# Kernel optimization log

Measured on AMD Instinct MI355X. Metric: run time of the kernel, lower is better.

Reference implementation:

```python
import jax, jax.numpy as jnp
import numpy as np

B = 2048
TT_IN = (16, 16, 16)    # prod = 4096
TT_OUT = (16, 16, 16)   # prod = 4096
BOND = (32, 32)
INIT_STD = 0.05  # keras 'random_normal' default stddev


def setup_inputs() -> dict:
    key = jax.random.key(0)
    k_x, k1, k2, k3 = jax.random.split(key, 4)
    x = jax.random.normal(k_x, (B, int(np.prod(TT_IN))), dtype=jnp.float32)
    core1 = jax.random.normal(k1, (TT_IN[0], TT_OUT[0], BOND[0]), dtype=jnp.float32) * INIT_STD
    core2 = jax.random.normal(k2, (TT_IN[1], TT_OUT[1], BOND[0], BOND[1]), dtype=jnp.float32) * INIT_STD
    core3 = jax.random.normal(k3, (TT_IN[2], TT_OUT[2], BOND[1]), dtype=jnp.float32) * INIT_STD
    bias = jnp.zeros(TT_OUT, dtype=jnp.float32)
    return {"x": x, "core1": core1, "core2": core2, "core3": core3, "bias": bias}


def reference(x, core1, core2, core3, bias):
    # x: [B, 4096] -> [B, x, y, z] tensor-train input modes
    xt = x.reshape((x.shape[0],) + TT_IN)
    # TT contraction: modes x,y,z contracted with cores; a,b,c are output
    # modes; p,q are bond indices (matches original einsum structure for
    # 3 cores: x[1,2,3], c1[1,4,7], c2[2,5,7,8], c3[3,6,8] -> [4,5,6]).
    out = jnp.einsum('nxyz,xap,ybpq,zcq->nabc', xt, core1, core2, core3,
                     optimize='optimal')
    out = out + bias  # bias broadcast over batch, shape TT_OUT
    out = out.reshape(x.shape[0], -1)  # [B, prod(TT_OUT)]
    return jax.nn.relu(out)
```

## Files before the change

kernel.cpp:

```cpp
#include <hip/hip_runtime.h>
#include <hip/hip_bf16.h>
#include <stdint.h>


typedef short bf16x8 __attribute__((ext_vector_type(8)));
typedef float f32x4  __attribute__((ext_vector_type(4)));

#define MB 2048
#define KD 4096
#define ND 4096
#define NT_K 64

__device__ __forceinline__ unsigned short f32_bf16(float f) {
  union { float f; uint32_t u; } v; v.f = f;
  return (unsigned short)((v.u + 0x7fffu + ((v.u >> 16) & 1u)) >> 16);
}
__device__ __forceinline__ float bf2f(unsigned short u) {
  union { uint32_t i; float f; } v; v.i = ((uint32_t)u) << 16; return v.f;
}

__global__ void k_conv(const float* __restrict__ x, unsigned short* __restrict__ xb) {
  int i = blockIdx.x * 256 + threadIdx.x;
  const float4* x4 = (const float4*)x;
  float4 a = x4[2*i];
  float4 b = x4[2*i+1];
  ushort4 lo, hi;
  lo.x = f32_bf16(a.x); lo.y = f32_bf16(a.y); lo.z = f32_bf16(a.z); lo.w = f32_bf16(a.w);
  hi.x = f32_bf16(b.x); hi.y = f32_bf16(b.y); hi.z = f32_bf16(b.z); hi.w = f32_bf16(b.w);
  ushort4* o = (ushort4*)xb;
  o[2*i]   = lo;
  o[2*i+1] = hi;
}

__global__ __launch_bounds__(256) void k_wt(const float* __restrict__ c1,
                                            const float* __restrict__ c2,
                                            const float* __restrict__ c3,
                                            unsigned short* __restrict__ Wt) {
  __shared__ unsigned short sh[17472];
  int ab = blockIdx.x;
  int t = threadIdx.x;
  int a = ab >> 4, b = ab & 15;
  unsigned short* c2s = sh;
  float* c1s = (float*)(sh + 16448);

  #pragma unroll
  for (int y = 0; y < 16; ++y) {
    float4 v = *(const float4*)(c2 + (size_t)(y*16 + b)*1024 + t*4);
    ushort4 s;
    s.x = f32_bf16(v.x); s.y = f32_bf16(v.y); s.z = f32_bf16(v.z); s.w = f32_bf16(v.w);
    *(ushort4*)(c2s + y*1028 + t*4) = s;
  }
  c1s[t]       = c1[((t>>5)*16 + a)*32 + (t&31)];
  c1s[t+256]   = c1[(((t>>5)+8)*16 + a)*32 + (t&31)];
  __syncthreads();

  int xx = t >> 4, yy = t & 15;
  const float* c1r = c1s + xx*32;
  const unsigned short* c2r = c2s + yy*1028;
  float acc[32];
  #pragma unroll
  for (int q = 0; q < 32; ++q) acc[q] = 0.f;
  #pragma unroll 8
  for (int p = 0; p < 32; ++p) {
    float w = c1r[p];
    #pragma unroll
    for (int j = 0; j < 8; ++j) {
      ushort4 v = *(const ushort4*)(c2r + p*32 + j*4);
      acc[4*j+0] = fmaf(w, bf2f(v.x), acc[4*j+0]);
      acc[4*j+1] = fmaf(w, bf2f(v.y), acc[4*j+1]);
      acc[4*j+2] = fmaf(w, bf2f(v.z), acc[4*j+2]);
      acc[4*j+3] = fmaf(w, bf2f(v.w), acc[4*j+3]);
    }
  }
  __syncthreads();

  unsigned short* T2s  = sh;
  unsigned short* c3ps = sh + 8192;

  #pragma unroll
  for (int j = 0; j < 8; ++j) {
    ushort4 s;
    s.x = f32_bf16(acc[4*j+0]); s.y = f32_bf16(acc[4*j+1]);
    s.z = f32_bf16(acc[4*j+2]); s.w = f32_bf16(acc[4*j+3]);
    *(ushort4*)(T2s + t*32 + j*4) = s;
  }
  #pragma unroll
  for (int r = 0; r < 8; ++r) {
    int i4 = t*8 + r;
    float4 v = *(const float4*)(c3 + (size_t)i4*4);
    int e = i4*4;
    int q = e & 31, zc = e >> 5;
    int z = zc >> 4, c = zc & 15;
    ushort4 s;
    s.x = f32_bf16(v.x); s.y = f32_bf16(v.y); s.z = f32_bf16(v.z); s.w = f32_bf16(v.w);
    *(ushort4*)(c3ps + (c*16 + z)*32 + q) = s;
  }
  __syncthreads();

  int wid = t >> 6, lane = t & 63, l15 = lane & 15, lg = lane >> 4;
  bf16x8 bfv[16];
  #pragma unroll
  for (int nt = 0; nt < 16; ++nt)
    bfv[nt] = *(const bf16x8*)(c3ps + (nt*16 + l15)*32 + lg*8);
  #pragma unroll
  for (int mi = 0; mi < 4; ++mi) {
    int mtile = wid*4 + mi;
    bf16x8 af = *(const bf16x8*)(T2s + (mtile*16 + l15)*32 + lg*8);
    #pragma unroll
    for (int nt = 0; nt < 16; ++nt) {
      f32x4 d = {0.f, 0.f, 0.f, 0.f};
      d = __builtin_amdgcn_mfma_f32_16x16x32_bf16(af, bfv[nt], d, 0, 0, 0);
      size_t jrow = (size_t)(ab*16 + nt) * ND;
      #pragma unroll
      for (int i = 0; i < 4; ++i) {
        int xy = mtile*16 + lg*4 + i;
        Wt[jrow + xy*16 + l15] = f32_bf16(d[i]);
      }
    }
  }
}

__device__ __forceinline__ void gload_lds16(const unsigned short* g, unsigned short* l) {
  __builtin_amdgcn_global_load_lds(
      (const __attribute__((address_space(1))) void*)g,
      (__attribute__((address_space(3))) void*)l, 16, 0, 0);
}

__global__ __launch_bounds__(512, 1) void k_gemm(const unsigned short* __restrict__ A,
                                                 const unsigned short* __restrict__ Bw,
                                                 const float* __restrict__ bias,
                                                 float* __restrict__ C) {
  __shared__ unsigned short As[3*128*64];
  __shared__ unsigned short Bs[3*256*64];
  const int t = threadIdx.x;
  const int wid = t >> 6, lane = t & 63;
  const int l15 = lane & 15, lg = lane >> 4;
  const int m0 = blockIdx.y * 128;
  const int n0 = blockIdx.x * 256;
  const int wr = wid >> 2, wc = wid & 3;
  const int xr = l15 & 7;

  const int scol = (((t & 7) ^ ((t >> 3) & 7)) * 8);
  const int t8 = t * 8;
  const unsigned short* Ag = A  + (size_t)(m0 + (t >> 3))*KD + scol;
  const unsigned short* Bg = Bw + (size_t)(n0 + (t >> 3))*KD + scol;

#define STG_A(tk, buf, s) gload_lds16(Ag + (size_t)(s)*64*KD + (tk)*64, \
                                      As + (buf)*8192  + (s)*4096 + t8)
#define STG_B(tk, buf, s) gload_lds16(Bg + (size_t)(s)*64*KD + (tk)*64, \
                                      Bs + (buf)*16384 + (s)*4096 + t8)

  f32x4 acc[4][4];
  #pragma unroll
  for (int m = 0; m < 4; ++m)
    #pragma unroll
    for (int n = 0; n < 4; ++n)
      acc[m][n] = (f32x4){0.f, 0.f, 0.f, 0.f};

  STG_A(0,0,0); STG_A(0,0,1); STG_B(0,0,0); STG_B(0,0,1); STG_B(0,0,2); STG_B(0,0,3);
  STG_A(1,1,0); STG_A(1,1,1); STG_B(1,1,0); STG_B(1,1,1); STG_B(1,1,2); STG_B(1,1,3);
  asm volatile("s_waitcnt vmcnt(6)" ::: "memory");
  __builtin_amdgcn_s_barrier();

  int cur = 0, stg = 2;
  for (int i = 0; i < NT_K; ++i) {
    const unsigned short* Ac = As + cur*8192;
    const unsigned short* Bc = Bs + cur*16384;
    const int  tk2 = i + 2;
    const bool do_stage = (i < NT_K - 2);
    bf16x8 aF[4], bF[4];

    {
      const int pc8 = ((0*4 + lg) ^ xr) * 8;
      #pragma unroll
      for (int m = 0; m < 4; ++m)
        aF[m] = *(const bf16x8*)(Ac + (wr*64 + m*16 + l15)*64 + pc8);
      #pragma unroll
      for (int n = 0; n < 4; ++n)
        bF[n] = *(const bf16x8*)(Bc + (wc*64 + n*16 + l15)*64 + pc8);
    }
    if (do_stage) { STG_A(tk2, stg, 0); STG_A(tk2, stg, 1); STG_B(tk2, stg, 0); }
    __builtin_amdgcn_s_barrier();
    asm volatile("s_waitcnt lgkmcnt(0)" ::: "memory");
    __builtin_amdgcn_sched_barrier(0);
    __builtin_amdgcn_s_setprio(1);
    #pragma unroll
    for (int m = 0; m < 4; ++m)
      #pragma unroll
      for (int n = 0; n < 4; ++n)
        acc[m][n] = __builtin_amdgcn_mfma_f32_16x16x32_bf16(aF[m], bF[n], acc[m][n], 0, 0, 0);
    __builtin_amdgcn_s_setprio(0);
    __builtin_amdgcn_s_barrier();

    {
      const int pc8 = ((1*4 + lg) ^ xr) * 8;
      #pragma unroll
      for (int m = 0; m < 4; ++m)
        aF[m] = *(const bf16x8*)(Ac + (wr*64 + m*16 + l15)*64 + pc8);
      #pragma unroll
      for (int n = 0; n < 4; ++n)
        bF[n] = *(const bf16x8*)(Bc + (wc*64 + n*16 + l15)*64 + pc8);
    }
    if (do_stage) { STG_B(tk2, stg, 1); STG_B(tk2, stg, 2); STG_B(tk2, stg, 3); }
    __builtin_amdgcn_s_barrier();
    asm volatile("s_waitcnt lgkmcnt(0)" ::: "memory");
    __builtin_amdgcn_sched_barrier(0);
    __builtin_amdgcn_s_setprio(1);
    #pragma unroll
    for (int m = 0; m < 4; ++m)
      #pragma unroll
      for (int n = 0; n < 4; ++n)
        acc[m][n] = __builtin_amdgcn_mfma_f32_16x16x32_bf16(aF[m], bF[n], acc[m][n], 0, 0, 0);
    __builtin_amdgcn_s_setprio(0);

    if (i < NT_K - 2)       { asm volatile("s_waitcnt vmcnt(6)" ::: "memory"); }
    else if (i == NT_K - 2) { asm volatile("s_waitcnt vmcnt(0)" ::: "memory"); }
    __builtin_amdgcn_s_barrier();

    cur = (cur == 2) ? 0 : cur + 1;
    stg = (stg == 2) ? 0 : stg + 1;
  }

  #pragma unroll
  for (int m = 0; m < 4; ++m) {
    int gr = m0 + wr*64 + m*16 + lg*4;
    #pragma unroll
    for (int n = 0; n < 4; ++n) {
      int gc = n0 + wc*64 + n*16 + l15;
      float bv = bias[gc];
      #pragma unroll
      for (int i = 0; i < 4; ++i) {
        float v = acc[m][n][i] + bv;
        C[(size_t)(gr + i)*ND + gc] = v > 0.f ? v : 0.f;
      }
    }
  }
#undef STG_A
#undef STG_B
}

extern "C" void kernel_launch(void* const* d_in, const int* in_sizes, int n_in,
                              void* d_out, int out_size, void* d_ws, size_t ws_size,
                              hipStream_t stream) {
  (void)in_sizes; (void)n_in; (void)out_size; (void)ws_size;
  const float* x    = (const float*)d_in[0];
  const float* c1   = (const float*)d_in[1];
  const float* c2   = (const float*)d_in[2];
  const float* c3   = (const float*)d_in[3];
  const float* bias = (const float*)d_in[4];
  float* out = (float*)d_out;

  uint8_t* ws = (uint8_t*)d_ws;
  unsigned short* xb = (unsigned short*)(ws);
  unsigned short* Wt = (unsigned short*)(ws + 16777216);

  k_conv<<<4096, 256, 0, stream>>>(x, xb);
  k_wt  <<<256,  256, 0, stream>>>(c1, c2, c3, Wt);
  k_gemm<<<dim3(ND/256, MB/128), 512, 0, stream>>>(xb, Wt, bias, out);
}
```

Baseline: 171.7 us.

## Split K across wave pairs in GEMM with LDS reduction of partial sums

```diff
diff --git a/kernel.cpp b/kernel.cpp
--- a/kernel.cpp
+++ b/kernel.cpp
@@ -130,14 +130,16 @@
                                                  const unsigned short* __restrict__ Bw,
                                                  const float* __restrict__ bias,
                                                  float* __restrict__ C) {
-  __shared__ unsigned short As[3*128*64];
-  __shared__ unsigned short Bs[3*256*64];
+  __shared__ uint8_t sh[147456];
+  unsigned short* As = (unsigned short*)sh;
+  unsigned short* Bs = (unsigned short*)(sh + 49152);
   const int t = threadIdx.x;
   const int wid = t >> 6, lane = t & 63;
   const int l15 = lane & 15, lg = lane >> 4;
   const int m0 = blockIdx.y * 128;
   const int n0 = blockIdx.x * 256;
-  const int wr = wid >> 2, wc = wid & 3;
+  const int wc  = wid & 3;
+  const int kkw = wid >> 2;
   const int xr = l15 & 7;
 
   const int scol = (((t & 7) ^ ((t >> 3) & 7)) * 8);
@@ -150,9 +152,9 @@
 #define STG_B(tk, buf, s) gload_lds16(Bg + (size_t)(s)*64*KD + (tk)*64, \
                                       Bs + (buf)*16384 + (s)*4096 + t8)
 
-  f32x4 acc[4][4];
-  #pragma unroll
-  for (int m = 0; m < 4; ++m)
+  f32x4 acc[8][4];
+  #pragma unroll
+  for (int m = 0; m < 8; ++m)
     #pragma unroll
     for (int n = 0; n < 4; ++n)
       acc[m][n] = (f32x4){0.f, 0.f, 0.f, 0.f};
@@ -162,76 +164,66 @@
   asm volatile("s_waitcnt vmcnt(6)" ::: "memory");
   __builtin_amdgcn_s_barrier();
 
+  const int pc8 = ((kkw*4 + lg) ^ xr) * 8;
+
   int cur = 0, stg = 2;
   for (int i = 0; i < NT_K; ++i) {
     const unsigned short* Ac = As + cur*8192;
     const unsigned short* Bc = Bs + cur*16384;
-    const int  tk2 = i + 2;
-    const bool do_stage = (i < NT_K - 2);
-    bf16x8 aF[4], bF[4];
-
-    {
-      const int pc8 = ((0*4 + lg) ^ xr) * 8;
-      #pragma unroll
-      for (int m = 0; m < 4; ++m)
-        aF[m] = *(const bf16x8*)(Ac + (wr*64 + m*16 + l15)*64 + pc8);
-      #pragma unroll
-      for (int n = 0; n < 4; ++n)
-        bF[n] = *(const bf16x8*)(Bc + (wc*64 + n*16 + l15)*64 + pc8);
-    }
-    if (do_stage) { STG_A(tk2, stg, 0); STG_A(tk2, stg, 1); STG_B(tk2, stg, 0); }
-    __builtin_amdgcn_s_barrier();
+    bf16x8 aF[8], bF[4];
+    #pragma unroll
+    for (int m = 0; m < 8; ++m)
+      aF[m] = *(const bf16x8*)(Ac + (m*16 + l15)*64 + pc8);
+    #pragma unroll
+    for (int n = 0; n < 4; ++n)
+      bF[n] = *(const bf16x8*)(Bc + (wc*64 + n*16 + l15)*64 + pc8);
+    if (i < NT_K - 2) {
+      const int tk2 = i + 2;
+      STG_A(tk2, stg, 0); STG_A(tk2, stg, 1);
+      STG_B(tk2, stg, 0); STG_B(tk2, stg, 1); STG_B(tk2, stg, 2); STG_B(tk2, stg, 3);
+    }
     asm volatile("s_waitcnt lgkmcnt(0)" ::: "memory");
     __builtin_amdgcn_sched_barrier(0);
     __builtin_amdgcn_s_setprio(1);
     #pragma unroll
-    for (int m = 0; m < 4; ++m)
+    for (int m = 0; m < 8; ++m)
       #pragma unroll
       for (int n = 0; n < 4; ++n)
         acc[m][n] = __builtin_amdgcn_mfma_f32_16x16x32_bf16(aF[m], bF[n], acc[m][n], 0, 0, 0);
     __builtin_amdgcn_s_setprio(0);
-    __builtin_amdgcn_s_barrier();
-
-    {
-      const int pc8 = ((1*4 + lg) ^ xr) * 8;
-      #pragma unroll
-      for (int m = 0; m < 4; ++m)
-        aF[m] = *(const bf16x8*)(Ac + (wr*64 + m*16 + l15)*64 + pc8);
-      #pragma unroll
-      for (int n = 0; n < 4; ++n)
-        bF[n] = *(const bf16x8*)(Bc + (wc*64 + n*16 + l15)*64 + pc8);
-    }
-    if (do_stage) { STG_B(tk2, stg, 1); STG_B(tk2, stg, 2); STG_B(tk2, stg, 3); }
-    __builtin_amdgcn_s_barrier();
-    asm volatile("s_waitcnt lgkmcnt(0)" ::: "memory");
-    __builtin_amdgcn_sched_barrier(0);
-    __builtin_amdgcn_s_setprio(1);
-    #pragma unroll
-    for (int m = 0; m < 4; ++m)
-      #pragma unroll
-      for (int n = 0; n < 4; ++n)
-        acc[m][n] = __builtin_amdgcn_mfma_f32_16x16x32_bf16(aF[m], bF[n], acc[m][n], 0, 0, 0);
-    __builtin_amdgcn_s_setprio(0);
-
     if (i < NT_K - 2)       { asm volatile("s_waitcnt vmcnt(6)" ::: "memory"); }
     else if (i == NT_K - 2) { asm volatile("s_waitcnt vmcnt(0)" ::: "memory"); }
     __builtin_amdgcn_s_barrier();
-
     cur = (cur == 2) ? 0 : cur + 1;
     stg = (stg == 2) ? 0 : stg + 1;
   }
 
-  #pragma unroll
-  for (int m = 0; m < 4; ++m) {
-    int gr = m0 + wr*64 + m*16 + lg*4;
-    #pragma unroll
-    for (int n = 0; n < 4; ++n) {
-      int gc = n0 + wc*64 + n*16 + l15;
-      float bv = bias[gc];
-      #pragma unroll
-      for (int i = 0; i < 4; ++i) {
-        float v = acc[m][n][i] + bv;
-        C[(size_t)(gr + i)*ND + gc] = v > 0.f ? v : 0.f;
+  __syncthreads();
+  float* mrg = (float*)sh;
+  if (kkw == 1) {
+    float* base = mrg + wc*8192;
+    #pragma unroll
+    for (int m = 0; m < 8; ++m)
+      #pragma unroll
+      for (int n = 0; n < 4; ++n)
+        *(f32x4*)(base + ((m*4 + n)*64 + lane)*4) = acc[m][n];
+  }
+  __syncthreads();
+  if (kkw == 0) {
+    float* base = mrg + wc*8192;
+    #pragma unroll
+    for (int m = 0; m < 8; ++m) {
+      int gr = m0 + m*16 + lg*4;
+      #pragma unroll
+      for (int n = 0; n < 4; ++n) {
+        f32x4 o = *(const f32x4*)(base + ((m*4 + n)*64 + lane)*4);
+        int gc = n0 + wc*64 + n*16 + l15;
+        float bv = bias[gc];
+        #pragma unroll
+        for (int i = 0; i < 4; ++i) {
+          float v = acc[m][n][i] + o[i] + bv;
+          C[(size_t)(gr + i)*ND + gc] = v > 0.f ? v : 0.f;
+        }
       }
     }
   }
```

Result: faster. 163.5 us (-4.8%).
